# Kernel tuning notes

Hardware: AMD Instinct MI355X
Metric: run time of the kernel (lower is better)

Reference implementation:

```python
import jax, jax.numpy as jnp
import numpy as np

N_HEADS = 16
R = 64  # number of latents; note: scale = r**-0.5 per original code


def setup_inputs() -> dict:
    key = jax.random.key(0)
    ks = jax.random.split(key, 8)
    B, S, D = 32, 4096, 1024
    s = D ** -0.5
    return {
        "x": jax.random.normal(ks[0], (B, S, D), dtype=jnp.float32),
        "wq": jax.random.normal(ks[1], (D, D), dtype=jnp.float32) * s,
        "kv_latent": jax.random.normal(ks[2], (R, D), dtype=jnp.float32),
        "wo": jax.random.normal(ks[3], (D, D), dtype=jnp.float32) * s,
        "w1": jax.random.normal(ks[4], (D, D), dtype=jnp.float32) * s,
        "b1": jnp.zeros((D,), dtype=jnp.float32),
        "w2": jax.random.normal(ks[5], (D, D), dtype=jnp.float32) * s,
        "b2": jnp.zeros((D,), dtype=jnp.float32),
    }


def reference(x, wq, kv_latent, wo, w1, b1, w2, b2):
    B, S, D = x.shape
    hd = D // N_HEADS
    scale = R ** -0.5
    q = x.reshape(-1, D)                                   # [N, D], N = B*S
    xq = (q @ wq).reshape(-1, N_HEADS, hd) * scale         # [N, H, hd]
    kv = kv_latent.reshape(R, N_HEADS, hd)                 # [R, H, hd]
    attn = jax.nn.softmax(jnp.einsum('nhd,rhd->nhr', xq, kv), axis=-1)
    out = jnp.einsum('nhr,rhd->nhd', attn, kv).reshape(-1, D)
    out = out @ wo                                         # [N, D]
    # residual MLP block (exact GELU, matching torch nn.GELU default)
    h = jax.nn.gelu(out @ w1 + b1, approximate=False)
    out = h @ w2 + b2 + out
    # mean-pool per segment; equal segments of length S -> equivalent to
    # block_diag(ones(l)/l) @ out without materializing the [B, N] mask
    return out.reshape(B, S, D).mean(axis=1)               # [B, D]
```

## Files before the change

### kernel.cpp

```cpp
#include <hip/hip_runtime.h>

using bf16x8 = __attribute__((ext_vector_type(8))) __bf16;
using f32x4  = __attribute__((ext_vector_type(4))) float;

#define AS1(p) ((const __attribute__((address_space(1))) void*)(p))
#define AS3(p) ((__attribute__((address_space(3))) void*)(p))

__device__ __forceinline__ unsigned short f2bf(float f) {
  unsigned u = __float_as_uint(f);
  u += 0x7fffu + ((u >> 16) & 1u);
  return (unsigned short)(u >> 16);
}
__device__ __forceinline__ float bf2f(unsigned short h) {
  return __uint_as_float(((unsigned)h) << 16);
}

__global__ __launch_bounds__(256) void convert_weights(
    const float* __restrict__ wq, const float* __restrict__ wo,
    const float* __restrict__ w1, const float* __restrict__ w2,
    const float* __restrict__ kv,
    unsigned short* __restrict__ wqT, unsigned short* __restrict__ woT,
    unsigned short* __restrict__ w1T, unsigned short* __restrict__ w2T,
    unsigned short* __restrict__ kvb, unsigned short* __restrict__ kvT) {
  int idx = blockIdx.x * 256 + threadIdx.x;
  int n = idx >> 10, k = idx & 1023;
  int src = k * 1024 + n;
  wqT[idx] = f2bf(wq[src]);
  woT[idx] = f2bf(wo[src]);
  w1T[idx] = f2bf(w1[src]);
  w2T[idx] = f2bf(w2[src]);
  if (idx < 65536) {
    kvb[idx] = f2bf(kv[idx]);
    int h = idx >> 12, d = (idx >> 6) & 63, r = idx & 63;
    kvT[idx] = f2bf(kv[r * 1024 + h * 64 + d]);
  }
}

template <int EPI, bool AF32>
__global__ __launch_bounds__(256) void gemm128(
    const void* __restrict__ Ap, const unsigned short* __restrict__ BT,
    unsigned short* __restrict__ C, const float* __restrict__ bias,
    const unsigned short* __restrict__ resid, float* __restrict__ pool,
    float scale) {
  __shared__ unsigned short As[128 * 32];
  __shared__ unsigned short Bs[128 * 32];
  const int tid = threadIdx.x;
  const int lane = tid & 63, wave = tid >> 6;
  const int wr = wave >> 1, wc = wave & 1;
  const int l15 = lane & 15, l4 = lane >> 4;
  const int row0 = blockIdx.y * 128, col0 = blockIdx.x * 128;

  f32x4 acc[4][4];
#pragma unroll
  for (int i = 0; i < 4; i++)
#pragma unroll
    for (int j = 0; j < 4; j++) acc[i][j] = f32x4{0.f, 0.f, 0.f, 0.f};

  for (int k0 = 0; k0 < 1024; k0 += 32) {
    if (AF32) {
      const float* A = (const float*)Ap;
#pragma unroll
      for (int s = 0; s < 4; s++) {
        int c = tid + 256 * s;
        int r = c >> 3, c4 = c & 7;
        const float4 v = *(const float4*)(A + (size_t)(row0 + r) * 1024 + k0 + c4 * 4);
        ushort4 b;
        b.x = f2bf(v.x); b.y = f2bf(v.y); b.z = f2bf(v.z); b.w = f2bf(v.w);
        *(ushort4*)(As + c * 4) = b;
      }
    } else {
      const unsigned short* A = (const unsigned short*)Ap;
#pragma unroll
      for (int t = 0; t < 2; t++) {
        int c = wave * 128 + t * 64 + lane;
        int r = c >> 2, c8 = c & 3;
        __builtin_amdgcn_global_load_lds(AS1(A + (size_t)(row0 + r) * 1024 + k0 + c8 * 8),
                                         AS3(As + (wave * 128 + t * 64) * 8), 16, 0, 0);
      }
    }
#pragma unroll
    for (int t = 0; t < 2; t++) {
      int c = wave * 128 + t * 64 + lane;
      int r = c >> 2, c8 = c & 3;
      __builtin_amdgcn_global_load_lds(AS1(BT + (size_t)(col0 + r) * 1024 + k0 + c8 * 8),
                                       AS3(Bs + (wave * 128 + t * 64) * 8), 16, 0, 0);
    }
    __syncthreads();

    bf16x8 af[4], bfr[4];
#pragma unroll
    for (int i = 0; i < 4; i++)
      af[i] = *(const bf16x8*)(As + (wr * 64 + i * 16 + l15) * 32 + l4 * 8);
#pragma unroll
    for (int j = 0; j < 4; j++)
      bfr[j] = *(const bf16x8*)(Bs + (wc * 64 + j * 16 + l15) * 32 + l4 * 8);
#pragma unroll
    for (int i = 0; i < 4; i++)
#pragma unroll
      for (int j = 0; j < 4; j++)
        acc[i][j] = __builtin_amdgcn_mfma_f32_16x16x32_bf16(af[i], bfr[j], acc[i][j], 0, 0, 0);
    __syncthreads();
  }

  if (EPI == 0) {
#pragma unroll
    for (int i = 0; i < 4; i++)
#pragma unroll
      for (int j = 0; j < 4; j++)
#pragma unroll
        for (int v = 0; v < 4; v++) {
          int row = row0 + wr * 64 + i * 16 + l4 * 4 + v;
          int col = col0 + wc * 64 + j * 16 + l15;
          C[(size_t)row * 1024 + col] = f2bf(acc[i][j][v] * scale);
        }
  } else if (EPI == 1) {
#pragma unroll
    for (int j = 0; j < 4; j++) {
      int col = col0 + wc * 64 + j * 16 + l15;
      float bj = bias[col];
#pragma unroll
      for (int i = 0; i < 4; i++)
#pragma unroll
        for (int v = 0; v < 4; v++) {
          int row = row0 + wr * 64 + i * 16 + l4 * 4 + v;
          float val = acc[i][j][v] + bj;
          float g = 0.5f * val * (1.0f + erff(val * 0.70710678118654752f));
          C[(size_t)row * 1024 + col] = f2bf(g);
        }
    }
  } else {
    float cs[4] = {0.f, 0.f, 0.f, 0.f};
#pragma unroll
    for (int j = 0; j < 4; j++) {
      int col = col0 + wc * 64 + j * 16 + l15;
      float bj = bias[col];
#pragma unroll
      for (int i = 0; i < 4; i++)
#pragma unroll
        for (int v = 0; v < 4; v++) {
          int row = row0 + wr * 64 + i * 16 + l4 * 4 + v;
          float val = acc[i][j][v] + bj + bf2f(resid[(size_t)row * 1024 + col]);
          cs[j] += val;
        }
    }
#pragma unroll
    for (int j = 0; j < 4; j++) {
      cs[j] += __shfl_xor(cs[j], 16);
      cs[j] += __shfl_xor(cs[j], 32);
    }
    if (l4 == 0) {
      int b = row0 >> 12;
#pragma unroll
      for (int j = 0; j < 4; j++) {
        int col = col0 + wc * 64 + j * 16 + l15;
        atomicAdd(pool + b * 1024 + col, cs[j] * (1.0f / 4096.0f));
      }
    }
  }
}

__global__ __launch_bounds__(256) void attn_kernel(
    const unsigned short* __restrict__ q, const unsigned short* __restrict__ kvb,
    const unsigned short* __restrict__ kvT, unsigned short* __restrict__ outp) {
  __shared__ unsigned short smem[32768];
  unsigned short* qs   = smem;
  unsigned short* kvs  = smem + 16384;
  unsigned short* kvTs = smem + 24576;
  const int tid = threadIdx.x;
  const int lane = tid & 63, wave = tid >> 6;
  const int wr = wave >> 1, wc = wave & 1;
  const int l15 = lane & 15, l4 = lane >> 4;
  const int hp = blockIdx.x, row0 = blockIdx.y * 128;

#pragma unroll
  for (int t = 0; t < 8; t++) {
    int c = wave * 512 + t * 64 + lane;
    int r = c >> 4, c8 = c & 15;
    __builtin_amdgcn_global_load_lds(AS1(q + (size_t)(row0 + r) * 1024 + hp * 128 + c8 * 8),
                                     AS3(qs + (wave * 512 + t * 64) * 8), 16, 0, 0);
  }
#pragma unroll
  for (int t = 0; t < 4; t++) {
    int c = wave * 256 + t * 64 + lane;
    int h = c >> 9, r = (c >> 3) & 63, c8 = c & 7;
    __builtin_amdgcn_global_load_lds(AS1(kvb + r * 1024 + (hp * 2 + h) * 64 + c8 * 8),
                                     AS3(kvs + (wave * 256 + t * 64) * 8), 16, 0, 0);
    __builtin_amdgcn_global_load_lds(AS1(kvT + (hp * 2 + h) * 4096 + (c & 511) * 8),
                                     AS3(kvTs + (wave * 256 + t * 64) * 8), 16, 0, 0);
  }
  __syncthreads();

  f32x4 sc[4][4];
#pragma unroll
  for (int i = 0; i < 4; i++)
#pragma unroll
    for (int j = 0; j < 4; j++) sc[i][j] = f32x4{0.f, 0.f, 0.f, 0.f};
#pragma unroll
  for (int ks = 0; ks < 2; ks++) {
    bf16x8 af[4], bfr[4];
#pragma unroll
    for (int i = 0; i < 4; i++)
      af[i] = *(const bf16x8*)(qs + (wr * 64 + i * 16 + l15) * 128 + wc * 64 + ks * 32 + l4 * 8);
#pragma unroll
    for (int j = 0; j < 4; j++)
      bfr[j] = *(const bf16x8*)(kvs + wc * 4096 + (j * 16 + l15) * 64 + ks * 32 + l4 * 8);
#pragma unroll
    for (int i = 0; i < 4; i++)
#pragma unroll
      for (int j = 0; j < 4; j++)
        sc[i][j] = __builtin_amdgcn_mfma_f32_16x16x32_bf16(af[i], bfr[j], sc[i][j], 0, 0, 0);
  }
  __syncthreads();

  unsigned short* attn = qs;
#pragma unroll
  for (int i = 0; i < 4; i++)
#pragma unroll
    for (int v = 0; v < 4; v++) {
      float m = fmaxf(fmaxf(sc[i][0][v], sc[i][1][v]), fmaxf(sc[i][2][v], sc[i][3][v]));
#pragma unroll
      for (int msk = 1; msk <= 8; msk <<= 1) m = fmaxf(m, __shfl_xor(m, msk));
      float e0 = __expf(sc[i][0][v] - m), e1 = __expf(sc[i][1][v] - m);
      float e2 = __expf(sc[i][2][v] - m), e3 = __expf(sc[i][3][v] - m);
      float s = e0 + e1 + e2 + e3;
#pragma unroll
      for (int msk = 1; msk <= 8; msk <<= 1) s += __shfl_xor(s, msk);
      float inv = 1.0f / s;
      int row = wr * 64 + i * 16 + l4 * 4 + v;
      attn[wc * 8192 + row * 64 + 0 * 16 + l15] = f2bf(e0 * inv);
      attn[wc * 8192 + row * 64 + 1 * 16 + l15] = f2bf(e1 * inv);
      attn[wc * 8192 + row * 64 + 2 * 16 + l15] = f2bf(e2 * inv);
      attn[wc * 8192 + row * 64 + 3 * 16 + l15] = f2bf(e3 * inv);
    }

  f32x4 o[4][4];
#pragma unroll
  for (int i = 0; i < 4; i++)
#pragma unroll
    for (int j = 0; j < 4; j++) o[i][j] = f32x4{0.f, 0.f, 0.f, 0.f};
#pragma unroll
  for (int ks = 0; ks < 2; ks++) {
    bf16x8 af[4], bfr[4];
#pragma unroll
    for (int i = 0; i < 4; i++)
      af[i] = *(const bf16x8*)(attn + wc * 8192 + (wr * 64 + i * 16 + l15) * 64 + ks * 32 + l4 * 8);
#pragma unroll
    for (int j = 0; j < 4; j++)
      bfr[j] = *(const bf16x8*)(kvTs + wc * 4096 + (j * 16 + l15) * 64 + ks * 32 + l4 * 8);
#pragma unroll
    for (int i = 0; i < 4; i++)
#pragma unroll
      for (int j = 0; j < 4; j++)
        o[i][j] = __builtin_amdgcn_mfma_f32_16x16x32_bf16(af[i], bfr[j], o[i][j], 0, 0, 0);
  }
#pragma unroll
  for (int i = 0; i < 4; i++)
#pragma unroll
    for (int j = 0; j < 4; j++)
#pragma unroll
      for (int v = 0; v < 4; v++) {
        int row = row0 + wr * 64 + i * 16 + l4 * 4 + v;
        int col = (hp * 2 + wc) * 64 + j * 16 + l15;
        outp[(size_t)row * 1024 + col] = f2bf(o[i][j][v]);
      }
}

extern "C" void kernel_launch(void* const* d_in, const int* in_sizes, int n_in,
                              void* d_out, int out_size, void* d_ws, size_t ws_size,
                              hipStream_t stream) {
  const float* x  = (const float*)d_in[0];
  const float* wq = (const float*)d_in[1];
  const float* kv = (const float*)d_in[2];
  const float* wo = (const float*)d_in[3];
  const float* w1 = (const float*)d_in[4];
  const float* b1 = (const float*)d_in[5];
  const float* w2 = (const float*)d_in[6];
  const float* b2 = (const float*)d_in[7];
  char* ws = (char*)d_ws;
  const size_t MB = 1024 * 1024;
  unsigned short* wqT = (unsigned short*)(ws + 0 * MB);
  unsigned short* woT = (unsigned short*)(ws + 2 * MB);
  unsigned short* w1T = (unsigned short*)(ws + 4 * MB);
  unsigned short* w2T = (unsigned short*)(ws + 6 * MB);
  unsigned short* kvb = (unsigned short*)(ws + 8 * MB);
  unsigned short* kvT = (unsigned short*)(ws + 8 * MB + 256 * 1024);
  unsigned short* buf1 = (unsigned short*)(ws + 16 * MB);
  unsigned short* buf2 = (unsigned short*)(ws + 16 * MB + 256 * MB);
  float* out = (float*)d_out;

  hipMemsetAsync(d_out, 0, (size_t)out_size * sizeof(float), stream);
  convert_weights<<<4096, 256, 0, stream>>>(wq, wo, w1, w2, kv, wqT, woT, w1T, w2T, kvb, kvT);

  dim3 g(8, 1024);
  gemm128<0, true ><<<g, 256, 0, stream>>>(x, wqT, buf1, nullptr, nullptr, nullptr, 0.125f);
  attn_kernel<<<g, 256, 0, stream>>>(buf1, kvb, kvT, buf2);
  gemm128<0, false><<<g, 256, 0, stream>>>(buf2, woT, buf1, nullptr, nullptr, nullptr, 1.0f);
  gemm128<1, false><<<g, 256, 0, stream>>>(buf1, w1T, buf2, b1, nullptr, nullptr, 1.0f);
  gemm128<2, false><<<g, 256, 0, stream>>>(buf2, w2T, nullptr, b2, buf1, out, 1.0f);
}
```

Baseline: 2.631 ms.

## Swizzle GEMM LDS layout, remap blocks per XCD, and tile weight transpose

Applies an XOR swizzle to the 16-byte chunks of the A and B tiles in LDS so the MFMA fragment reads hit fewer bank conflicts. The GEMM blocks are also remapped so that each XCD handles a contiguous band of row tiles, which improves L2 reuse of A rows across the column tiles. The weight conversion becomes a shared-memory tiled transpose with coalesced reads and writes, and the kv conversion moves into its own small kernel. The swizzle has to match exactly on both the write and the read side.

New measurement: 2.442 ms. 1.08x faster.

```diff
diff --git a/kernel.cpp b/kernel.cpp
--- a/kernel.cpp
+++ b/kernel.cpp
@@ -15,25 +15,37 @@
   return __uint_as_float(((unsigned)h) << 16);
 }
 
-__global__ __launch_bounds__(256) void convert_weights(
+__global__ __launch_bounds__(256) void transpose_w(
     const float* __restrict__ wq, const float* __restrict__ wo,
     const float* __restrict__ w1, const float* __restrict__ w2,
-    const float* __restrict__ kv,
     unsigned short* __restrict__ wqT, unsigned short* __restrict__ woT,
-    unsigned short* __restrict__ w1T, unsigned short* __restrict__ w2T,
-    unsigned short* __restrict__ kvb, unsigned short* __restrict__ kvT) {
+    unsigned short* __restrict__ w1T, unsigned short* __restrict__ w2T) {
+  __shared__ float tile[64][65];
+  const int z = blockIdx.z;
+  const float* src = z == 0 ? wq : z == 1 ? wo : z == 2 ? w1 : w2;
+  unsigned short* dst = z == 0 ? wqT : z == 1 ? woT : z == 2 ? w1T : w2T;
+  const int tx = threadIdx.x & 63, ty = threadIdx.x >> 6;
+  const int n0 = blockIdx.x * 64, k0 = blockIdx.y * 64;
+#pragma unroll
+  for (int i = 0; i < 16; i++) {
+    int k = ty * 16 + i;
+    tile[k][tx] = src[(size_t)(k0 + k) * 1024 + n0 + tx];
+  }
+  __syncthreads();
+#pragma unroll
+  for (int i = 0; i < 16; i++) {
+    int n = ty * 16 + i;
+    dst[(size_t)(n0 + n) * 1024 + k0 + tx] = f2bf(tile[tx][n]);
+  }
+}
+
+__global__ __launch_bounds__(256) void convert_kv(
+    const float* __restrict__ kv, unsigned short* __restrict__ kvb,
+    unsigned short* __restrict__ kvT) {
   int idx = blockIdx.x * 256 + threadIdx.x;
-  int n = idx >> 10, k = idx & 1023;
-  int src = k * 1024 + n;
-  wqT[idx] = f2bf(wq[src]);
-  woT[idx] = f2bf(wo[src]);
-  w1T[idx] = f2bf(w1[src]);
-  w2T[idx] = f2bf(w2[src]);
-  if (idx < 65536) {
-    kvb[idx] = f2bf(kv[idx]);
-    int h = idx >> 12, d = (idx >> 6) & 63, r = idx & 63;
-    kvT[idx] = f2bf(kv[r * 1024 + h * 64 + d]);
-  }
+  kvb[idx] = f2bf(kv[idx]);
+  int h = idx >> 12, d = (idx >> 6) & 63, r = idx & 63;
+  kvT[idx] = f2bf(kv[r * 1024 + h * 64 + d]);
 }
 
 template <int EPI, bool AF32>
@@ -48,13 +60,17 @@
   const int lane = tid & 63, wave = tid >> 6;
   const int wr = wave >> 1, wc = wave & 1;
   const int l15 = lane & 15, l4 = lane >> 4;
-  const int row0 = blockIdx.y * 128, col0 = blockIdx.x * 128;
+  const int bid = blockIdx.y * 8 + blockIdx.x;
+  const int xcd = bid & 7, j = bid >> 3;
+  const int row0 = ((xcd << 7) | (j >> 3)) * 128;
+  const int col0 = (j & 7) * 128;
+  const int swz = (l15 >> 1) & 3;
 
   f32x4 acc[4][4];
 #pragma unroll
   for (int i = 0; i < 4; i++)
 #pragma unroll
-    for (int j = 0; j < 4; j++) acc[i][j] = f32x4{0.f, 0.f, 0.f, 0.f};
+    for (int jj = 0; jj < 4; jj++) acc[i][jj] = f32x4{0.f, 0.f, 0.f, 0.f};
 
   for (int k0 = 0; k0 < 1024; k0 += 32) {
     if (AF32) {
@@ -66,39 +82,40 @@
         const float4 v = *(const float4*)(A + (size_t)(row0 + r) * 1024 + k0 + c4 * 4);
         ushort4 b;
         b.x = f2bf(v.x); b.y = f2bf(v.y); b.z = f2bf(v.z); b.w = f2bf(v.w);
-        *(ushort4*)(As + c * 4) = b;
+        int cc = (c4 >> 1) ^ ((r >> 1) & 3), h = c4 & 1;
+        *(ushort4*)(As + r * 32 + cc * 8 + h * 4) = b;
       }
     } else {
       const unsigned short* A = (const unsigned short*)Ap;
 #pragma unroll
       for (int t = 0; t < 2; t++) {
-        int c = wave * 128 + t * 64 + lane;
-        int r = c >> 2, c8 = c & 3;
-        __builtin_amdgcn_global_load_lds(AS1(A + (size_t)(row0 + r) * 1024 + k0 + c8 * 8),
-                                         AS3(As + (wave * 128 + t * 64) * 8), 16, 0, 0);
+        int p = wave * 128 + t * 64 + lane;
+        int r = p >> 2, c = (p & 3) ^ ((r >> 1) & 3);
+        __builtin_amdgcn_global_load_lds(AS1(A + (size_t)(row0 + r) * 1024 + k0 + c * 8),
+                                         AS3(As + p * 8), 16, 0, 0);
       }
     }
 #pragma unroll
     for (int t = 0; t < 2; t++) {
-      int c = wave * 128 + t * 64 + lane;
-      int r = c >> 2, c8 = c & 3;
-      __builtin_amdgcn_global_load_lds(AS1(BT + (size_t)(col0 + r) * 1024 + k0 + c8 * 8),
-                                       AS3(Bs + (wave * 128 + t * 64) * 8), 16, 0, 0);
+      int p = wave * 128 + t * 64 + lane;
+      int r = p >> 2, c = (p & 3) ^ ((r >> 1) & 3);
+      __builtin_amdgcn_global_load_lds(AS1(BT + (size_t)(col0 + r) * 1024 + k0 + c * 8),
+                                       AS3(Bs + p * 8), 16, 0, 0);
     }
     __syncthreads();
 
     bf16x8 af[4], bfr[4];
 #pragma unroll
     for (int i = 0; i < 4; i++)
-      af[i] = *(const bf16x8*)(As + (wr * 64 + i * 16 + l15) * 32 + l4 * 8);
-#pragma unroll
-    for (int j = 0; j < 4; j++)
-      bfr[j] = *(const bf16x8*)(Bs + (wc * 64 + j * 16 + l15) * 32 + l4 * 8);
-#pragma unroll
-    for (int i = 0; i < 4; i++)
-#pragma unroll
-      for (int j = 0; j < 4; j++)
-        acc[i][j] = __builtin_amdgcn_mfma_f32_16x16x32_bf16(af[i], bfr[j], acc[i][j], 0, 0, 0);
+      af[i] = *(const bf16x8*)(As + (wr * 64 + i * 16 + l15) * 32 + (l4 ^ swz) * 8);
+#pragma unroll
+    for (int jj = 0; jj < 4; jj++)
+      bfr[jj] = *(const bf16x8*)(Bs + (wc * 64 + jj * 16 + l15) * 32 + (l4 ^ swz) * 8);
+#pragma unroll
+    for (int i = 0; i < 4; i++)
+#pragma unroll
+      for (int jj = 0; jj < 4; jj++)
+        acc[i][jj] = __builtin_amdgcn_mfma_f32_16x16x32_bf16(af[i], bfr[jj], acc[i][jj], 0, 0, 0);
     __syncthreads();
   }
 
@@ -106,24 +123,24 @@
 #pragma unroll
     for (int i = 0; i < 4; i++)
 #pragma unroll
-      for (int j = 0; j < 4; j++)
+      for (int jj = 0; jj < 4; jj++)
 #pragma unroll
         for (int v = 0; v < 4; v++) {
           int row = row0 + wr * 64 + i * 16 + l4 * 4 + v;
-          int col = col0 + wc * 64 + j * 16 + l15;
-          C[(size_t)row * 1024 + col] = f2bf(acc[i][j][v] * scale);
+          int col = col0 + wc * 64 + jj * 16 + l15;
+          C[(size_t)row * 1024 + col] = f2bf(acc[i][jj][v] * scale);
         }
   } else if (EPI == 1) {
 #pragma unroll
-    for (int j = 0; j < 4; j++) {
-      int col = col0 + wc * 64 + j * 16 + l15;
+    for (int jj = 0; jj < 4; jj++) {
+      int col = col0 + wc * 64 + jj * 16 + l15;
       float bj = bias[col];
 #pragma unroll
       for (int i = 0; i < 4; i++)
 #pragma unroll
         for (int v = 0; v < 4; v++) {
           int row = row0 + wr * 64 + i * 16 + l4 * 4 + v;
-          float val = acc[i][j][v] + bj;
+          float val = acc[i][jj][v] + bj;
           float g = 0.5f * val * (1.0f + erff(val * 0.70710678118654752f));
           C[(size_t)row * 1024 + col] = f2bf(g);
         }
@@ -131,29 +148,29 @@
   } else {
     float cs[4] = {0.f, 0.f, 0.f, 0.f};
 #pragma unroll
-    for (int j = 0; j < 4; j++) {
-      int col = col0 + wc * 64 + j * 16 + l15;
+    for (int jj = 0; jj < 4; jj++) {
+      int col = col0 + wc * 64 + jj * 16 + l15;
       float bj = bias[col];
 #pragma unroll
       for (int i = 0; i < 4; i++)
 #pragma unroll
         for (int v = 0; v < 4; v++) {
           int row = row0 + wr * 64 + i * 16 + l4 * 4 + v;
-          float val = acc[i][j][v] + bj + bf2f(resid[(size_t)row * 1024 + col]);
-          cs[j] += val;
+          float val = acc[i][jj][v] + bj + bf2f(resid[(size_t)row * 1024 + col]);
+          cs[jj] += val;
         }
     }
 #pragma unroll
-    for (int j = 0; j < 4; j++) {
-      cs[j] += __shfl_xor(cs[j], 16);
-      cs[j] += __shfl_xor(cs[j], 32);
+    for (int jj = 0; jj < 4; jj++) {
+      cs[jj] += __shfl_xor(cs[jj], 16);
+      cs[jj] += __shfl_xor(cs[jj], 32);
     }
     if (l4 == 0) {
       int b = row0 >> 12;
 #pragma unroll
-      for (int j = 0; j < 4; j++) {
-        int col = col0 + wc * 64 + j * 16 + l15;
-        atomicAdd(pool + b * 1024 + col, cs[j] * (1.0f / 4096.0f));
+      for (int jj = 0; jj < 4; jj++) {
+        int col = col0 + wc * 64 + jj * 16 + l15;
+        atomicAdd(pool + b * 1024 + col, cs[jj] * (1.0f / 4096.0f));
       }
     }
   }
@@ -289,7 +306,8 @@
   float* out = (float*)d_out;
 
   hipMemsetAsync(d_out, 0, (size_t)out_size * sizeof(float), stream);
-  convert_weights<<<4096, 256, 0, stream>>>(wq, wo, w1, w2, kv, wqT, woT, w1T, w2T, kvb, kvT);
+  transpose_w<<<dim3(16, 16, 4), 256, 0, stream>>>(wq, wo, w1, w2, wqT, woT, w1T, w2T);
+  convert_kv<<<256, 256, 0, stream>>>(kv, kvb, kvT);
 
   dim3 g(8, 1024);
   gemm128<0, true ><<<g, 256, 0, stream>>>(x, wqT, buf1, nullptr, nullptr, nullptr, 0.125f);
```
